# Kernel tuning notes

Measured on AMD Instinct MI355X. Metric: run time of the kernel, lower is better.

## Reference

```python
import jax, jax.numpy as jnp
import numpy as np

EPS = 1e-5
NEG = jnp.float32(-1e30)


def _mha(q_in, kv, in_w, in_b, out_w, out_b, n_heads, allowed=None):
    # torch nn.MultiheadAttention (batch_first, eval mode)
    B, Nq, D = q_in.shape
    hd = D // n_heads
    wq, wk, wv = jnp.split(in_w, 3, axis=0)
    bq, bk, bv = jnp.split(in_b, 3)
    q = (q_in @ wq.T + bq).reshape(B, Nq, n_heads, hd).transpose(0, 2, 1, 3)
    k = (kv @ wk.T + bk).reshape(B, -1, n_heads, hd).transpose(0, 2, 1, 3)
    v = (kv @ wv.T + bv).reshape(B, -1, n_heads, hd).transpose(0, 2, 1, 3)
    s = jnp.einsum('bhqd,bhkd->bhqk', q, k) / jnp.sqrt(jnp.float32(hd))
    if allowed is not None:
        s = jnp.where(allowed[:, None, :, :], s, NEG)
    a = jax.nn.softmax(s, axis=-1)
    o = jnp.einsum('bhqk,bhkd->bhqd', a, v).transpose(0, 2, 1, 3).reshape(B, Nq, D)
    o = o @ out_w.T + out_b
    if allowed is not None:
        # rows with no allowed keys: torch would NaN; we zero them (deterministic)
        o = jnp.where(allowed.any(-1)[..., None], o, 0.0)
    return o


def _layernorm(x, g, b):
    mu = x.mean(-1, keepdims=True)
    var = ((x - mu) ** 2).mean(-1, keepdims=True)
    return (x - mu) * jax.lax.rsqrt(var + EPS) * g + b


def setup_inputs() -> dict:
    key = jax.random.key(0)
    B, N, D, NH = 128, 128, 512, 8
    ks = jax.random.split(key, 16)
    s = 0.02
    return {
        'H': jax.random.normal(ks[0], (B, N, D), jnp.float32),
        'pred_heads': jax.random.randint(ks[1], (B, N), 0, N, jnp.int32),
        'mask': jnp.ones((B, N), jnp.int32),
        'head_in_w': jax.random.normal(ks[2], (3 * D, D)) * s,
        'head_in_b': jnp.zeros((3 * D,), jnp.float32),
        'head_out_w': jax.random.normal(ks[3], (D, D)) * s,
        'head_out_b': jnp.zeros((D,), jnp.float32),
        'sib_in_w': jax.random.normal(ks[4], (3 * D, D)) * s,
        'sib_in_b': jnp.zeros((3 * D,), jnp.float32),
        'sib_out_w': jax.random.normal(ks[5], (D, D)) * s,
        'sib_out_b': jnp.zeros((D,), jnp.float32),
        'child_w': jax.random.normal(ks[6], (D, 2 * D)) * s,
        'child_b': jnp.zeros((D,), jnp.float32),
        'gate_w': jax.random.normal(ks[7], (D, 4 * D)) * s,
        'gate_b': jnp.zeros((D,), jnp.float32),
        'trans_w': jax.random.normal(ks[8], (D, 4 * D)) * s,
        'trans_b': jnp.zeros((D,), jnp.float32),
        'ln_g': jnp.ones((D,), jnp.float32),
        'ln_b': jnp.zeros((D,), jnp.float32),
    }


def reference(H, pred_heads, mask, head_in_w, head_in_b, head_out_w, head_out_b,
              sib_in_w, sib_in_b, sib_out_w, sib_out_b, child_w, child_b,
              gate_w, gate_b, trans_w, trans_b, ln_g, ln_b):
    B, N, D = H.shape
    NH = 8
    heads = jnp.clip(pred_heads, 0, N - 1)  # [B,N]
    maskb = mask.astype(bool)

    # 1) head message: gather each node's head repr, attend Q=H, K=V=head_repr
    head_repr = jnp.take_along_axis(H, heads[..., None], axis=1)  # [B,N,D]
    head_msg = _mha(H, head_repr, head_in_w, head_in_b, head_out_w, head_out_b, NH)

    # 2) child aggregation: vectorized scatter-add replacing the Python loop.
    # loop runs d in [1, length) with mask a prefix -> valid = mask & (d >= 1)
    valid = maskb & (jnp.arange(N) >= 1)  # [B,N]
    contrib = H * valid[..., None].astype(H.dtype)
    flat_idx = (jnp.arange(B)[:, None] * N + heads).reshape(-1)
    child_sum = jnp.zeros((B * N, D), H.dtype).at[flat_idx].add(
        contrib.reshape(B * N, D)).reshape(B, N, D)
    child_count = jnp.zeros((B * N,), H.dtype).at[flat_idx].add(
        valid.reshape(-1).astype(H.dtype)).reshape(B, N, 1)
    child_avg = child_sum / jnp.maximum(child_count, 1.0)
    child_msg = jax.nn.gelu(
        jnp.concatenate([H, child_avg], -1) @ child_w.T + child_b,
        approximate=False)

    # 3) sibling attention (N <= 128 branch): same head, not self, both masked-in
    same_head = heads[:, :, None] == heads[:, None, :]
    eye = jnp.eye(N, dtype=bool)[None]
    allowed = same_head & ~eye & maskb[:, None, :] & maskb[:, :, None]
    sib_msg = _mha(H, H, sib_in_w, sib_in_b, sib_out_w, sib_out_b, NH, allowed=allowed)

    # 4) gated fusion + residual + layernorm
    combined = jnp.concatenate([H, head_msg, child_msg, sib_msg], -1)
    gate = jax.nn.sigmoid(combined @ gate_w.T + gate_b)
    update = jax.nn.gelu(combined @ trans_w.T + trans_b, approximate=False)
    return _layernorm(H + gate * update, ln_g, ln_b)
```

## Files before the change

### kernel.cpp

```cpp
#include <hip/hip_runtime.h>
#include <hip/hip_bf16.h>

typedef __bf16 bf16x8 __attribute__((ext_vector_type(8)));
typedef float f32x4 __attribute__((ext_vector_type(4)));

__device__ __forceinline__ void gload16(const void* g, void* l) {
  __builtin_amdgcn_global_load_lds(
      (const __attribute__((address_space(1))) unsigned int*)g,
      (__attribute__((address_space(3))) unsigned int*)l, 16, 0, 0);
}

__device__ __forceinline__ float gelu_f(float x) {
  return 0.5f * x * (1.f + erff(x * 0.70710678118654752f));
}
__device__ __forceinline__ float sigmoid_f(float x) {
  return 1.f / (1.f + __expf(-x));
}

template<int EPI>
__global__ __launch_bounds__(512, 2)
void gemm8_kernel(const __hip_bfloat16* __restrict__ A0, int lda0,
                  const __hip_bfloat16* __restrict__ A1, int lda1,
                  const __hip_bfloat16* __restrict__ A2, int lda2,
                  int ks1, int ks2,
                  const __hip_bfloat16* __restrict__ B, int ldb,
                  const float* __restrict__ bias,
                  const float* __restrict__ fvec,
                  const float* __restrict__ flags,
                  void* __restrict__ C, int ldc, int K)
{
  extern __shared__ __align__(16) char lds[];
  const int t = threadIdx.x;
  const int l = t & 63;
  const int w = t >> 6;
  const int l15 = l & 15, lg = (l >> 4) & 3;
  const int orig = blockIdx.y * gridDim.x + blockIdx.x;
  const int nwg = gridDim.x * gridDim.y;
  const int gy = gridDim.y;
  const int xcd = orig & 7, rk = orig >> 3, q = nwg >> 3, r = nwg & 7;
  const int bid = (xcd < r ? xcd * (q + 1) : r * (q + 1) + (xcd - r) * q) + rk;
  const int m0 = (bid % gy) * 256;
  const int n0 = (bid / gy) * 256;

  const int srow = t >> 2;
  const int kc8 = ((t & 3) ^ ((t >> 3) & 3)) * 8;
  const int mbase = (w >> 2) * 128;
  const int nbase = (w & 3) * 64;
  const int swz = (l15 >> 1) & 3;
  const int kslot = (lg ^ swz) * 8;
  int aoff[8], boff[4];
#pragma unroll
  for (int mf = 0; mf < 8; ++mf) aoff[mf] = (mbase + mf * 16 + l15) * 32 + kslot;
#pragma unroll
  for (int nf = 0; nf < 4; ++nf) boff[nf] = (nbase + nf * 16 + l15) * 32 + kslot;

  auto segA = [&](int k0, const __hip_bfloat16*& Ap, int& ldA, int& krel) {
    if (k0 >= ks2)      { Ap = A2; ldA = lda2; krel = k0 - ks2; }
    else if (k0 >= ks1) { Ap = A1; ldA = lda1; krel = k0 - ks1; }
    else                { Ap = A0; ldA = lda0; krel = k0; }
  };
  auto stageA = [&](int buf, const __hip_bfloat16* Ap, int ldA, int krel) {
    char* base = lds + buf * 32768 + t * 16;
    gload16(Ap + (size_t)(m0 + srow) * ldA + krel + kc8, base);
    gload16(Ap + (size_t)(m0 + 128 + srow) * ldA + krel + kc8, base + 8192);
  };
  auto stageB = [&](int buf, int k0) {
    char* base = lds + buf * 32768 + 16384 + t * 16;
    gload16(B + (size_t)(n0 + srow) * ldb + k0 + kc8, base);
    gload16(B + (size_t)(n0 + 128 + srow) * ldb + k0 + kc8, base + 8192);
  };

  f32x4 acc[8][4] = {};
  const int NT = K >> 5;

#pragma unroll 1
  for (int pt = 0; pt < 3; ++pt) {
    const __hip_bfloat16* Ap; int ldA, krel;
    segA(pt * 32, Ap, ldA, krel);
    stageA(pt, Ap, ldA, krel);
    stageB(pt, pt * 32);
  }
  asm volatile("s_waitcnt vmcnt(8)" ::: "memory");
  __builtin_amdgcn_s_barrier();
  __builtin_amdgcn_sched_barrier(0);

#pragma unroll 1
  for (int tt = 0; tt < NT; ++tt) {
    const int buf = tt & 3;
    const __hip_bfloat16* As = (const __hip_bfloat16*)(lds + buf * 32768);
    const __hip_bfloat16* Bs = (const __hip_bfloat16*)(lds + buf * 32768 + 16384);
    const int pf = tt + 3;
    const bool do_pf = pf < NT;
    const int pbuf = pf & 3;
    const __hip_bfloat16* Ap = A0; int ldA = lda0, krel = 0;
    if (do_pf) segA(pf * 32, Ap, ldA, krel);

    bf16x8 bv[4], av[4];
#pragma unroll
    for (int nf = 0; nf < 4; ++nf) bv[nf] = *(const bf16x8*)(Bs + boff[nf]);
#pragma unroll
    for (int mf = 0; mf < 4; ++mf) av[mf] = *(const bf16x8*)(As + aoff[mf]);
    if (do_pf) stageA(pbuf, Ap, ldA, krel);
    __builtin_amdgcn_s_setprio(1);
#pragma unroll
    for (int mf = 0; mf < 4; ++mf)
#pragma unroll
      for (int nf = 0; nf < 4; ++nf)
        acc[mf][nf] = __builtin_amdgcn_mfma_f32_16x16x32_bf16(av[mf], bv[nf], acc[mf][nf], 0, 0, 0);
    __builtin_amdgcn_s_setprio(0);

#pragma unroll
    for (int mf = 0; mf < 4; ++mf) av[mf] = *(const bf16x8*)(As + aoff[mf + 4]);
    if (do_pf) stageB(pbuf, pf * 32);
    __builtin_amdgcn_s_setprio(1);
#pragma unroll
    for (int mf = 0; mf < 4; ++mf)
#pragma unroll
      for (int nf = 0; nf < 4; ++nf)
        acc[mf + 4][nf] = __builtin_amdgcn_mfma_f32_16x16x32_bf16(av[mf], bv[nf], acc[mf + 4][nf], 0, 0, 0);
    __builtin_amdgcn_s_setprio(0);

    __builtin_amdgcn_sched_barrier(0);
    if (tt + 3 < NT)      asm volatile("s_waitcnt vmcnt(8)" ::: "memory");
    else if (tt + 2 < NT) asm volatile("s_waitcnt vmcnt(4)" ::: "memory");
    else if (tt + 1 < NT) asm volatile("s_waitcnt vmcnt(0)" ::: "memory");
    if (tt + 1 < NT) {
      __builtin_amdgcn_s_barrier();
      __builtin_amdgcn_sched_barrier(0);
    }
  }

  if (EPI == 2) {
#pragma unroll
    for (int mf = 0; mf < 8; ++mf) {
#pragma unroll
      for (int nh = 0; nh < 2; ++nh) {
        const int nf = nh * 2;
        const int sc = n0 + nbase + nf * 16;
        const float bg = bias[sc + l15], bt = bias[sc + 16 + l15];
        const float fg = fvec[sc + l15], ft = fvec[sc + 16 + l15];
        const int ocol = (sc >> 5) * 16 + l15;
#pragma unroll
        for (int j = 0; j < 4; ++j) {
          const int row = m0 + mbase + mf * 16 + lg * 4 + j;
          const float flg = flags[row];
          float g  = acc[mf][nf][j]     + bg + flg * fg;
          float tv = acc[mf][nf + 1][j] + bt + flg * ft;
          ((__hip_bfloat16*)C)[(size_t)row * ldc + ocol] =
              __float2bfloat16(sigmoid_f(g) * gelu_f(tv));
        }
      }
    }
    return;
  }
#pragma unroll
  for (int mf = 0; mf < 8; ++mf)
#pragma unroll
    for (int nf = 0; nf < 4; ++nf) {
      const int col = n0 + nbase + nf * 16 + l15;
      const float bc = bias ? bias[col] : 0.f;
#pragma unroll
      for (int j = 0; j < 4; ++j) {
        const int row = m0 + mbase + mf * 16 + lg * 4 + j;
        ((__hip_bfloat16*)C)[(size_t)row * ldc + col] =
            __float2bfloat16(acc[mf][nf][j] + bc);
      }
    }
}

template<int EPI, bool OBF16>
__global__ __launch_bounds__(256)
void gemm_kernel(const __hip_bfloat16* __restrict__ A0, int lda0,
                 const __hip_bfloat16* __restrict__ A1, int lda1,
                 const __hip_bfloat16* __restrict__ A2, int lda2,
                 int ks1, int ks2,
                 const __hip_bfloat16* __restrict__ B, int ldb,
                 const float* __restrict__ bias,
                 const float* __restrict__ fvec,
                 const float* __restrict__ flags,
                 void* __restrict__ C, int ldc, int K)
{
  __shared__ __align__(16) __hip_bfloat16 As[128 * 32];
  __shared__ __align__(16) __hip_bfloat16 Bs[128 * 32];
  const int t = threadIdx.x;
  const int l = t & 63, w = t >> 6;
  const int gx = gridDim.x;
  int bid = blockIdx.y * gx + blockIdx.x;
  {
    const int nwg = gx * gridDim.y;
    const int xcd = bid & 7, rk = bid >> 3, q = nwg >> 3, r = nwg & 7;
    bid = (xcd < r ? xcd * (q + 1) : r * (q + 1) + (xcd - r) * q) + rk;
  }
  const int m0 = (bid / gx) * 128, n0 = (bid % gx) * 128;
  const int wm = (w >> 1) * 64, wn = (w & 1) * 64;
  const int l15 = l & 15, lg = l >> 4;

  const int r0 = t >> 2;
  const int kk0 = ((t & 3) ^ ((t >> 3) & 3)) * 8;
  char* lA = (char*)As + t * 16;
  char* lB = (char*)Bs + t * 16;
  const size_t boff1 = (size_t)(n0 + r0) * ldb + kk0;
  const size_t boff2 = (size_t)(n0 + r0 + 64) * ldb + kk0;

  int aoffR[4], boffR[4];
#pragma unroll
  for (int i = 0; i < 4; ++i) {
    const int ra = wm + i * 16 + l15;
    aoffR[i] = ra * 32 + ((lg ^ ((ra >> 1) & 3)) * 8);
    const int rb = wn + i * 16 + l15;
    boffR[i] = rb * 32 + ((lg ^ ((rb >> 1) & 3)) * 8);
  }
  f32x4 acc[4][4] = {};

#pragma unroll 1
  for (int seg = 0; seg < 3; ++seg) {
    const __hip_bfloat16* Ap;
    int ldA, kb, ke;
    if (seg == 0)      { Ap = A0; ldA = lda0; kb = 0;   ke = ks1; }
    else if (seg == 1) { Ap = A1; ldA = lda1; kb = ks1; ke = ks2; }
    else               { Ap = A2; ldA = lda2; kb = ks2; ke = K;   }
    if (kb >= ke) continue;
    const size_t aoff1 = (size_t)(m0 + r0) * ldA + kk0;
    const size_t aoff2 = (size_t)(m0 + r0 + 64) * ldA + kk0;
    for (int k0 = kb; k0 < ke; k0 += 32) {
      const int kr = k0 - kb;
      gload16(Ap + aoff1 + kr, lA);
      gload16(Ap + aoff2 + kr, lA + 4096);
      gload16(B + boff1 + k0, lB);
      gload16(B + boff2 + k0, lB + 4096);
      __syncthreads();
      bf16x8 af[4], bfr[4];
#pragma unroll
      for (int i = 0; i < 4; ++i) {
        af[i]  = *(const bf16x8*)((const __hip_bfloat16*)As + aoffR[i]);
        bfr[i] = *(const bf16x8*)((const __hip_bfloat16*)Bs + boffR[i]);
      }
#pragma unroll
      for (int mi = 0; mi < 4; ++mi)
#pragma unroll
        for (int ni = 0; ni < 4; ++ni)
          acc[mi][ni] = __builtin_amdgcn_mfma_f32_16x16x32_bf16(af[mi], bfr[ni], acc[mi][ni], 0, 0, 0);
      __syncthreads();
    }
  }

#pragma unroll
  for (int mi = 0; mi < 4; ++mi)
#pragma unroll
    for (int ni = 0; ni < 4; ++ni) {
      const int col = n0 + wn + ni * 16 + l15;
      const float bc = bias ? bias[col] : 0.f;
#pragma unroll
      for (int j = 0; j < 4; ++j) {
        const int row = m0 + wm + mi * 16 + lg * 4 + j;
        float v = acc[mi][ni][j] + bc;
        if (EPI == 1) v = gelu_f(v);
        if (OBF16) ((__hip_bfloat16*)C)[(size_t)row * ldc + col] = __float2bfloat16(v);
        else       ((float*)C)[(size_t)row * ldc + col] = v;
      }
    }
}

__global__ __launch_bounds__(256)
void attn_kernel(const __hip_bfloat16* __restrict__ QKV,
                 const int* __restrict__ pred_heads,
                 const int* __restrict__ mask,
                 __hip_bfloat16* __restrict__ Oout,
                 float* __restrict__ flags)
{
  __shared__ __align__(16) __hip_bfloat16 smem[128 * 128];
  __shared__ __align__(16) __hip_bfloat16 Vt[64 * 128];
  __shared__ int hs[128];
  __shared__ int key[128];
  const bool SIB = blockIdx.x >= 1024;
  const int bh = blockIdx.x & 1023;
  const int b = bh >> 3, h = bh & 7;
  const int qofs = SIB ? 1536 : 0;
  __hip_bfloat16* Ob = Oout + (SIB ? 512 : 0);
  const int t = threadIdx.x, l = t & 63, w = t >> 6;
  const int l15 = l & 15, lg = l >> 4;
  __hip_bfloat16* Qs = smem;
  __hip_bfloat16* Ks = smem + 128 * 64;

  if (t < 128) {
    int hh = pred_heads[b * 128 + t];
    hh = hh < 0 ? 0 : (hh > 127 ? 127 : hh);
    hs[t] = hh;
    key[t] = mask[b * 128 + t] ? hh : (128 + t);
  }
  __syncthreads();
  const size_t tb = (size_t)b * 128 * 3072;
  const int co = qofs + h * 64;
#pragma unroll
  for (int it = 0; it < 4; ++it) {
    const int idx = it * 256 + t;
    const int row = idx >> 3;
    const int c8 = (idx & 7) * 8;
    const int sl = ((c8 >> 3) ^ (row & 7)) * 8;
    *(uint4*)(Qs + row * 64 + sl) = *(const uint4*)(QKV + tb + (size_t)row * 3072 + co + c8);
    const int krow = SIB ? row : hs[row];
    *(uint4*)(Ks + row * 64 + sl) = *(const uint4*)(QKV + tb + (size_t)krow * 3072 + co + 512 + c8);
    uint4 vv = *(const uint4*)(QKV + tb + (size_t)krow * 3072 + co + 1024 + c8);
    const __hip_bfloat16* vp = (const __hip_bfloat16*)&vv;
#pragma unroll
    for (int u = 0; u < 8; ++u) {
      const int d = c8 + u;
      Vt[d * 128 + (((row >> 3) ^ (d & 7)) * 8) + (row & 7)] = vp[u];
    }
  }
  __syncthreads();

  const int r0 = w * 32;
  const int x7 = l15 & 7;
  f32x4 s[8][2] = {};
#pragma unroll
  for (int ks = 0; ks < 2; ++ks) {
    const int sl = ((ks * 4 + lg) ^ x7) * 8;
    bf16x8 qb0 = *(const bf16x8*)(Qs + (r0 + l15) * 64 + sl);
    bf16x8 qb1 = *(const bf16x8*)(Qs + (r0 + 16 + l15) * 64 + sl);
#pragma unroll
    for (int kf = 0; kf < 8; ++kf) {
      bf16x8 ka = *(const bf16x8*)(Ks + (kf * 16 + l15) * 64 + sl);
      s[kf][0] = __builtin_amdgcn_mfma_f32_16x16x32_bf16(ka, qb0, s[kf][0], 0, 0, 0);
      s[kf][1] = __builtin_amdgcn_mfma_f32_16x16x32_bf16(ka, qb1, s[kf][1], 0, 0, 0);
    }
  }

  const float scale = 0.125f;
  int kq[2] = {0, 0};
  int4 kv[8];
  if (SIB) {
    kq[0] = key[r0 + l15];
    kq[1] = key[r0 + 16 + l15];
#pragma unroll
    for (int kf = 0; kf < 8; ++kf) kv[kf] = *(const int4*)&key[kf * 16 + lg * 4];
  }
  float invs[2];
#pragma unroll
  for (int qf = 0; qf < 2; ++qf) {
    const int q = r0 + qf * 16 + l15;
    unsigned om = 0xFFFFFFFFu;
    if (SIB) {
      om = 0u;
#pragma unroll
      for (int kf = 0; kf < 8; ++kf) {
        const int* kp = (const int*)&kv[kf];
#pragma unroll
        for (int j = 0; j < 4; ++j) {
          const int k = kf * 16 + lg * 4 + j;
          if (kp[j] == kq[qf] && k != q) om |= (1u << (kf * 4 + j));
        }
      }
    }
    float mx = -1e30f;
#pragma unroll
    for (int kf = 0; kf < 8; ++kf)
#pragma unroll
      for (int j = 0; j < 4; ++j) {
        const float v = s[kf][qf][j] * scale;
        mx = fmaxf(mx, ((om >> (kf * 4 + j)) & 1u) ? v : -1e30f);
      }
    mx = fmaxf(mx, __shfl_xor(mx, 16));
    mx = fmaxf(mx, __shfl_xor(mx, 32));
    float sum = 0.f;
#pragma unroll
    for (int kf = 0; kf < 8; ++kf)
#pragma unroll
      for (int j = 0; j < 4; ++j) {
        const float v = s[kf][qf][j] * scale;
        const float p = ((om >> (kf * 4 + j)) & 1u) ? __expf(v - mx) : 0.f;
        s[kf][qf][j] = p;
        sum += p;
      }
    sum += __shfl_xor(sum, 16);
    sum += __shfl_xor(sum, 32);
    invs[qf] = sum > 0.f ? 1.f / sum : 0.f;
  }
  if (SIB && h == 0 && lg == 0) {
    flags[b * 128 + r0 + l15]      = invs[0] > 0.f ? 1.f : 0.f;
    flags[b * 128 + r0 + 16 + l15] = invs[1] > 0.f ? 1.f : 0.f;
  }

  __syncthreads();
#pragma unroll
  for (int qf = 0; qf < 2; ++qf) {
    const int q = r0 + qf * 16 + l15;
    const int base = q * 128 + ((lg & 1) << 2);
#pragma unroll
    for (int kf = 0; kf < 8; ++kf) {
      const int c16 = kf * 2 + (lg >> 1);
      __hip_bfloat16 pk[4];
#pragma unroll
      for (int j = 0; j < 4; ++j) pk[j] = __float2bfloat16(s[kf][qf][j] * invs[qf]);
      *(uint2*)(smem + base + ((c16 ^ x7) << 3)) = *(const uint2*)pk;
    }
  }
  __syncthreads();

  f32x4 o[2][4] = {};
#pragma unroll
  for (int js = 0; js < 4; ++js) {
    const int slp = ((js * 4 + lg) ^ x7) * 8;
    bf16x8 pa0 = *(const bf16x8*)(smem + (r0 + l15) * 128 + slp);
    bf16x8 pa1 = *(const bf16x8*)(smem + (r0 + 16 + l15) * 128 + slp);
#pragma unroll
    for (int dj = 0; dj < 4; ++dj) {
      bf16x8 vb = *(const bf16x8*)(Vt + (dj * 16 + l15) * 128 + slp);
      o[0][dj] = __builtin_amdgcn_mfma_f32_16x16x32_bf16(pa0, vb, o[0][dj], 0, 0, 0);
      o[1][dj] = __builtin_amdgcn_mfma_f32_16x16x32_bf16(pa1, vb, o[1][dj], 0, 0, 0);
    }
  }
  const int hb = h * 64;
#pragma unroll
  for (int mi = 0; mi < 2; ++mi)
#pragma unroll
    for (int dj = 0; dj < 4; ++dj)
#pragma unroll
      for (int j = 0; j < 4; ++j) {
        const int row = r0 + mi * 16 + lg * 4 + j;
        const int dc = dj * 16 + l15;
        Ob[(size_t)(b * 128 + row) * 1024 + hb + dc] = __float2bfloat16(o[mi][dj][j]);
      }
}

__global__ __launch_bounds__(256)
void child_kernel(const __hip_bfloat16* __restrict__ Hbf,
                  const int* __restrict__ pred_heads,
                  const int* __restrict__ mask,
                  __hip_bfloat16* __restrict__ Cavg)
{
  __shared__ float sum[128 * 64];
  __shared__ int cnt[128];
  __shared__ int hsl[128];
  __shared__ int vld[128];
  const int t = threadIdx.x;
  const int b = blockIdx.y, ch = blockIdx.x;
#pragma unroll
  for (int u = 0; u < 32; ++u) sum[u * 256 + t] = 0.f;
  if (t < 128) {
    int hh = pred_heads[b * 128 + t];
    hh = hh < 0 ? 0 : (hh > 127 ? 127 : hh);
    hsl[t] = hh;
    vld[t] = (mask[b * 128 + t] != 0) && (t >= 1);
    cnt[t] = 0;
  }
  __syncthreads();
  if (t < 128 && vld[t]) atomicAdd(&cnt[hsl[t]], 1);
  __syncthreads();
  const int c = t & 63;
  const int isub = t >> 6;
  for (int ii = 0; ii < 32; ++ii) {
    int i = ii * 4 + isub;
    if (vld[i])
      atomicAdd(&sum[hsl[i] * 64 + c],
                __bfloat162float(Hbf[((size_t)b * 128 + i) * 512 + ch * 64 + c]));
  }
  __syncthreads();
#pragma unroll
  for (int u = 0; u < 32; ++u) {
    int idx = u * 256 + t;
    int p = idx >> 6, cc = idx & 63;
    float avg = sum[idx] / fmaxf((float)cnt[p], 1.f);
    Cavg[((size_t)b * 128 + p) * 512 + ch * 64 + cc] = __float2bfloat16(avg);
  }
}

__global__ void prep_kernel(const float* __restrict__ hin_w, const float* __restrict__ sin_w,
                            const float* __restrict__ ch_w, const float* __restrict__ H,
                            __hip_bfloat16* __restrict__ Wqkv, __hip_bfloat16* __restrict__ Wch,
                            __hip_bfloat16* __restrict__ Hbf,
                            const float* __restrict__ gw, const float* __restrict__ tw,
                            const float* __restrict__ gb, const float* __restrict__ tb,
                            __hip_bfloat16* __restrict__ Wf, __hip_bfloat16* __restrict__ Whin,
                            __hip_bfloat16* __restrict__ Wsin, float* __restrict__ bias,
                            const float* __restrict__ hout_w, const float* __restrict__ sout_w,
                            __hip_bfloat16* __restrict__ WhoT, __hip_bfloat16* __restrict__ WsoT)
{
  int gid = blockIdx.x * 256 + threadIdx.x;
  if (gid < 2621440) {
    const float* s; __hip_bfloat16* d; int i;
    if      (gid <  196608) { s = hin_w; d = Wqkv;          i = gid; }
    else if (gid <  393216) { s = sin_w; d = Wqkv + 786432; i = gid - 196608; }
    else if (gid <  524288) { s = ch_w;  d = Wch;           i = gid - 393216; }
    else                    { s = H;     d = Hbf;           i = gid - 524288; }
    i *= 4;
    float4 v = *(const float4*)(s + i);
    union { __hip_bfloat16 h[4]; uint2 u; } p;
    p.h[0] = __float2bfloat16(v.x); p.h[1] = __float2bfloat16(v.y);
    p.h[2] = __float2bfloat16(v.z); p.h[3] = __float2bfloat16(v.w);
    *(uint2*)(d + i) = p.u;
  } else if (gid < 4718592) {
    int idx = gid - 2621440;
    int s = idx >> 11, c = idx & 2047;
    int q = s >> 5, r = s & 31;
    float v = (r < 16) ? gw[(size_t)(q * 16 + r) * 2048 + c]
                       : tw[(size_t)(q * 16 + r - 16) * 2048 + c];
    __hip_bfloat16 hv = __float2bfloat16(v);
    if      (c <  512) Wf[(size_t)s * 2048 + c] = hv;
    else if (c < 1024) Whin[(size_t)s * 512 + (c - 512)] = hv;
    else if (c < 1536) Wf[(size_t)s * 2048 + (c - 512)] = hv;
    else               Wsin[(size_t)s * 512 + (c - 1536)] = hv;
    if (c == 0) bias[s] = (r < 16) ? gb[q * 16 + r] : tb[q * 16 + r - 16];
  } else {
    int idx = gid - 4718592;
    const float* s = hout_w; __hip_bfloat16* d = WhoT;
    if (idx >= 262144) { s = sout_w; d = WsoT; idx -= 262144; }
    int i = idx >> 9, j = idx & 511;
    d[i * 512 + j] = __float2bfloat16(s[(size_t)j * 512 + i]);
  }
}

__global__ __launch_bounds__(256)
void foldbias_kernel(const __hip_bfloat16* __restrict__ Whin, const __hip_bfloat16* __restrict__ Wsin,
                     const float* __restrict__ hob, const float* __restrict__ sob,
                     float* __restrict__ bias_gt, float* __restrict__ fvec)
{
  const int s = blockIdx.x * 256 + threadIdx.x;
  float a = 0.f, c = 0.f;
  for (int j = 0; j < 512; j += 8) {
    bf16x8 wh = *(const bf16x8*)(Whin + (size_t)s * 512 + j);
    bf16x8 wsv = *(const bf16x8*)(Wsin + (size_t)s * 512 + j);
#pragma unroll
    for (int u = 0; u < 8; ++u) {
      a += (float)wh[u] * hob[j + u];
      c += (float)wsv[u] * sob[j + u];
    }
  }
  bias_gt[s] += a;
  fvec[s] = c;
}

__global__ __launch_bounds__(64)
void ln_kernel(const float* __restrict__ H, const __hip_bfloat16* __restrict__ U,
               const float* __restrict__ g, const float* __restrict__ bta,
               float* __restrict__ out)
{
  const int row = blockIdx.x, l = threadIdx.x;
  const size_t hb = (size_t)row * 512;
  const int c0 = l * 8;
  float4 h0 = *(const float4*)(H + hb + c0);
  float4 h1 = *(const float4*)(H + hb + c0 + 4);
  bf16x8 uv = *(const bf16x8*)(U + hb + c0);
  float x[8];
  x[0] = h0.x + (float)uv[0]; x[1] = h0.y + (float)uv[1];
  x[2] = h0.z + (float)uv[2]; x[3] = h0.w + (float)uv[3];
  x[4] = h1.x + (float)uv[4]; x[5] = h1.y + (float)uv[5];
  x[6] = h1.z + (float)uv[6]; x[7] = h1.w + (float)uv[7];
  float sum = 0.f;
#pragma unroll
  for (int u = 0; u < 8; ++u) sum += x[u];
#pragma unroll
  for (int m = 32; m; m >>= 1) sum += __shfl_xor(sum, m);
  const float mean = sum * (1.f / 512.f);
  float vs = 0.f;
#pragma unroll
  for (int u = 0; u < 8; ++u) { float d0 = x[u] - mean; vs += d0 * d0; }
#pragma unroll
  for (int m = 32; m; m >>= 1) vs += __shfl_xor(vs, m);
  const float rstd = rsqrtf(vs * (1.f / 512.f) + 1e-5f);
  float4 g0 = *(const float4*)(g + c0);
  float4 g1 = *(const float4*)(g + c0 + 4);
  float4 b0 = *(const float4*)(bta + c0);
  float4 b1 = *(const float4*)(bta + c0 + 4);
  float4 o0, o1;
  o0.x = (x[0] - mean) * rstd * g0.x + b0.x;
  o0.y = (x[1] - mean) * rstd * g0.y + b0.y;
  o0.z = (x[2] - mean) * rstd * g0.z + b0.z;
  o0.w = (x[3] - mean) * rstd * g0.w + b0.w;
  o1.x = (x[4] - mean) * rstd * g1.x + b1.x;
  o1.y = (x[5] - mean) * rstd * g1.y + b1.y;
  o1.z = (x[6] - mean) * rstd * g1.z + b1.z;
  o1.w = (x[7] - mean) * rstd * g1.w + b1.w;
  *(float4*)(out + hb + c0) = o0;
  *(float4*)(out + hb + c0 + 4) = o1;
}

extern "C" void kernel_launch(void* const* d_in, const int* in_sizes, int n_in,
                              void* d_out, int out_size, void* d_ws, size_t ws_size,
                              hipStream_t stream)
{
  (void)in_sizes; (void)n_in; (void)out_size; (void)ws_size;
  const float* H      = (const float*)d_in[0];
  const int*  pred    = (const int*)d_in[1];
  const int*  maskp   = (const int*)d_in[2];
  const float* hin_w  = (const float*)d_in[3];
  const float* hin_b  = (const float*)d_in[4];
  const float* hout_w = (const float*)d_in[5];
  const float* hout_b = (const float*)d_in[6];
  const float* sin_w  = (const float*)d_in[7];
  const float* sin_b  = (const float*)d_in[8];
  const float* sout_w = (const float*)d_in[9];
  const float* sout_b = (const float*)d_in[10];
  const float* ch_w   = (const float*)d_in[11];
  const float* ch_b   = (const float*)d_in[12];
  const float* g_w    = (const float*)d_in[13];
  const float* g_b    = (const float*)d_in[14];
  const float* t_w    = (const float*)d_in[15];
  const float* t_b    = (const float*)d_in[16];
  const float* lng    = (const float*)d_in[17];
  const float* lnb    = (const float*)d_in[18];

  char* ws = (char*)d_ws;
  __hip_bfloat16* Wqkv  = (__hip_bfloat16*)(ws + 0);
  __hip_bfloat16* Wch   = (__hip_bfloat16*)(ws + 3145728);
  __hip_bfloat16* Wgt   = (__hip_bfloat16*)(ws + 4194304);
  float* bias_qkv       = (float*)(ws + 8388608);
  float* bias_gt        = (float*)(ws + 8400896);
  float* fvec           = (float*)(ws + 8404992);
  float* flags          = (float*)(ws + 8409088);
  __hip_bfloat16* Hbf   = (__hip_bfloat16*)(ws + 8474624);
  char* QKVr            = ws + 25251840;
  __hip_bfloat16* QKV   = (__hip_bfloat16*)QKVr;
  __hip_bfloat16* Whin  = (__hip_bfloat16*)(QKVr + 0);
  __hip_bfloat16* Wsin  = (__hip_bfloat16*)(QKVr + 1048576);
  __hip_bfloat16* WhoT  = (__hip_bfloat16*)(QKVr + 2097152);
  __hip_bfloat16* WsoT  = (__hip_bfloat16*)(QKVr + 2621440);
  __hip_bfloat16* CHM   = (__hip_bfloat16*)(QKVr + 0);
  __hip_bfloat16* U     = (__hip_bfloat16*)(QKVr + 16777216);
  __hip_bfloat16* Cavg  = (__hip_bfloat16*)(QKVr + 50331648);
  __hip_bfloat16* CM2   = (__hip_bfloat16*)(ws + 125915136);

  hipFuncSetAttribute(reinterpret_cast<const void*>(gemm8_kernel<0>),
                      hipFuncAttributeMaxDynamicSharedMemorySize, 131072);
  hipFuncSetAttribute(reinterpret_cast<const void*>(gemm8_kernel<2>),
                      hipFuncAttributeMaxDynamicSharedMemorySize, 131072);

  prep_kernel<<<20480, 256, 0, stream>>>(hin_w, sin_w, ch_w, H, Wqkv, Wch, Hbf,
                                         g_w, t_w, g_b, t_b, Wgt, Whin, Wsin, bias_gt,
                                         hout_w, sout_w, WhoT, WsoT);
  foldbias_kernel<<<4, 256, 0, stream>>>(Whin, Wsin, hout_b, sout_b, bias_gt, fvec);
  hipMemcpyAsync(bias_qkv, hin_b, 1536 * 4, hipMemcpyDeviceToDevice, stream);
  hipMemcpyAsync(bias_qkv + 1536, sin_b, 1536 * 4, hipMemcpyDeviceToDevice, stream);

  gemm_kernel<0, true><<<dim3(4, 8), 256, 0, stream>>>(
      Whin, 512, Whin, 512, Whin, 512, 512, 512, WhoT, 512,
      (const float*)nullptr, (const float*)nullptr, (const float*)nullptr,
      (void*)(Wgt + 1024), 2048, 512);
  gemm_kernel<0, true><<<dim3(4, 8), 256, 0, stream>>>(
      Wsin, 512, Wsin, 512, Wsin, 512, 512, 512, WsoT, 512,
      (const float*)nullptr, (const float*)nullptr, (const float*)nullptr,
      (void*)(Wgt + 1536), 2048, 512);

  gemm8_kernel<0><<<dim3(12, 64), 512, 131072, stream>>>(
      Hbf, 512, Hbf, 512, Hbf, 512, 512, 512, Wqkv, 512,
      bias_qkv, (const float*)nullptr, (const float*)nullptr,
      (void*)QKV, 3072, 512);

  attn_kernel<<<2048, 256, 0, stream>>>(QKV, pred, maskp, CM2, flags);

  child_kernel<<<dim3(8, 128), 256, 0, stream>>>(Hbf, pred, maskp, Cavg);
  gemm_kernel<1, true><<<dim3(4, 128), 256, 0, stream>>>(
      Hbf, 512, Cavg, 512, Cavg, 512, 512, 1024, Wch, 1024,
      ch_b, (const float*)nullptr, (const float*)nullptr,
      (void*)CHM, 512, 1024);

  gemm8_kernel<2><<<dim3(4, 64), 512, 131072, stream>>>(
      Hbf, 512, CHM, 512, CM2, 1024, 512, 1024, Wgt, 2048,
      bias_gt, fvec, flags, (void*)U, 512, 2048);

  ln_kernel<<<16384, 64, 0, stream>>>(H, U, lng, lnb, (float*)d_out);
}
```

Baseline: 453.9 us.

## Restructure GEMM main loop into 64-wide K double-buffer with staged half-tile prefetch

```diff
diff --git a/kernel.cpp b/kernel.cpp
--- a/kernel.cpp
+++ b/kernel.cpp
@@ -41,66 +41,66 @@
   const int bid = (xcd < r ? xcd * (q + 1) : r * (q + 1) + (xcd - r) * q) + rk;
   const int m0 = (bid % gy) * 256;
   const int n0 = (bid / gy) * 256;
-
-  const int srow = t >> 2;
-  const int kc8 = ((t & 3) ^ ((t >> 3) & 3)) * 8;
-  const int mbase = (w >> 2) * 128;
-  const int nbase = (w & 3) * 64;
-  const int swz = (l15 >> 1) & 3;
-  const int kslot = (lg ^ swz) * 8;
-  int aoff[8], boff[4];
-#pragma unroll
-  for (int mf = 0; mf < 8; ++mf) aoff[mf] = (mbase + mf * 16 + l15) * 32 + kslot;
-#pragma unroll
-  for (int nf = 0; nf < 4; ++nf) boff[nf] = (nbase + nf * 16 + l15) * 32 + kslot;
+  const int wm = w >> 2, wn = w & 3;
+
+  const int srow0 = t >> 2;
+  const int sch = ((t & 3) ^ ((t >> 2) & 3)) * 8;
 
   auto segA = [&](int k0, const __hip_bfloat16*& Ap, int& ldA, int& krel) {
     if (k0 >= ks2)      { Ap = A2; ldA = lda2; krel = k0 - ks2; }
     else if (k0 >= ks1) { Ap = A1; ldA = lda1; krel = k0 - ks1; }
     else                { Ap = A0; ldA = lda0; krel = k0; }
   };
-  auto stageA = [&](int buf, const __hip_bfloat16* Ap, int ldA, int krel) {
-    char* base = lds + buf * 32768 + t * 16;
-    gload16(Ap + (size_t)(m0 + srow) * ldA + krel + kc8, base);
-    gload16(Ap + (size_t)(m0 + 128 + srow) * ldA + krel + kc8, base + 8192);
+  auto stageA = [&](int U, int kh) {
+    const __hip_bfloat16* Ap; int ldA, krel;
+    segA(U * 64 + kh * 32, Ap, ldA, krel);
+    char* dst = lds + (U & 1) * 65536 + kh * 16384 + t * 16;
+    gload16(Ap + (size_t)(m0 + srow0) * ldA + krel + sch, dst);
+    gload16(Ap + (size_t)(m0 + 128 + srow0) * ldA + krel + sch, dst + 8192);
   };
-  auto stageB = [&](int buf, int k0) {
-    char* base = lds + buf * 32768 + 16384 + t * 16;
-    gload16(B + (size_t)(n0 + srow) * ldb + k0 + kc8, base);
-    gload16(B + (size_t)(n0 + 128 + srow) * ldb + k0 + kc8, base + 8192);
+  auto stageB = [&](int U, int kh) {
+    const int k0 = U * 64 + kh * 32;
+    char* dst = lds + (U & 1) * 65536 + 32768 + kh * 16384 + t * 16;
+    gload16(B + (size_t)(n0 + srow0) * ldb + k0 + sch, dst);
+    gload16(B + (size_t)(n0 + 128 + srow0) * ldb + k0 + sch, dst + 8192);
   };
 
+  const int key = l15 & 3;
+  const int kch = (lg ^ key) * 8;
+  int aoff[8], boff[4];
+#pragma unroll
+  for (int mf = 0; mf < 8; ++mf) aoff[mf] = (wm * 128 + mf * 16 + l15) * 32 + kch;
+#pragma unroll
+  for (int nf = 0; nf < 4; ++nf) boff[nf] = (wn * 64 + nf * 16 + l15) * 32 + kch;
+
   f32x4 acc[8][4] = {};
-  const int NT = K >> 5;
-
-#pragma unroll 1
-  for (int pt = 0; pt < 3; ++pt) {
-    const __hip_bfloat16* Ap; int ldA, krel;
-    segA(pt * 32, Ap, ldA, krel);
-    stageA(pt, Ap, ldA, krel);
-    stageB(pt, pt * 32);
-  }
-  asm volatile("s_waitcnt vmcnt(8)" ::: "memory");
+  const int NT = K >> 6;
+
+  stageA(0, 0); stageB(0, 0); stageA(0, 1); stageB(0, 1);
+  if (NT > 1) { stageA(1, 0); stageB(1, 0); }
+  if (NT > 1) asm volatile("s_waitcnt vmcnt(8)" ::: "memory");
+  else        asm volatile("s_waitcnt vmcnt(4)" ::: "memory");
   __builtin_amdgcn_s_barrier();
   __builtin_amdgcn_sched_barrier(0);
 
 #pragma unroll 1
-  for (int tt = 0; tt < NT; ++tt) {
-    const int buf = tt & 3;
-    const __hip_bfloat16* As = (const __hip_bfloat16*)(lds + buf * 32768);
-    const __hip_bfloat16* Bs = (const __hip_bfloat16*)(lds + buf * 32768 + 16384);
-    const int pf = tt + 3;
-    const bool do_pf = pf < NT;
-    const int pbuf = pf & 3;
-    const __hip_bfloat16* Ap = A0; int ldA = lda0, krel = 0;
-    if (do_pf) segA(pf * 32, Ap, ldA, krel);
-
-    bf16x8 bv[4], av[4];
-#pragma unroll
-    for (int nf = 0; nf < 4; ++nf) bv[nf] = *(const bf16x8*)(Bs + boff[nf]);
-#pragma unroll
-    for (int mf = 0; mf < 4; ++mf) av[mf] = *(const bf16x8*)(As + aoff[mf]);
-    if (do_pf) stageA(pbuf, Ap, ldA, krel);
+  for (int U = 0; U < NT; ++U) {
+    const int b = U & 1;
+    const __hip_bfloat16* RA0 = (const __hip_bfloat16*)(lds + b * 65536);
+    const __hip_bfloat16* RA1 = (const __hip_bfloat16*)(lds + b * 65536 + 16384);
+    const __hip_bfloat16* RB0 = (const __hip_bfloat16*)(lds + b * 65536 + 32768);
+    const __hip_bfloat16* RB1 = (const __hip_bfloat16*)(lds + b * 65536 + 49152);
+    bf16x8 av[4], bv[4];
+
+#pragma unroll
+    for (int mf = 0; mf < 4; ++mf) av[mf] = *(const bf16x8*)(RA0 + aoff[mf]);
+#pragma unroll
+    for (int nf = 0; nf < 4; ++nf) bv[nf] = *(const bf16x8*)(RB0 + boff[nf]);
+    __builtin_amdgcn_sched_barrier(0);
+    if (U + 1 < NT) stageA(U + 1, 1);
+    __builtin_amdgcn_s_barrier();
+    asm volatile("s_waitcnt lgkmcnt(0)" ::: "memory");
+    __builtin_amdgcn_sched_barrier(0);
     __builtin_amdgcn_s_setprio(1);
 #pragma unroll
     for (int mf = 0; mf < 4; ++mf)
@@ -108,10 +108,15 @@
       for (int nf = 0; nf < 4; ++nf)
         acc[mf][nf] = __builtin_amdgcn_mfma_f32_16x16x32_bf16(av[mf], bv[nf], acc[mf][nf], 0, 0, 0);
     __builtin_amdgcn_s_setprio(0);
-
-#pragma unroll
-    for (int mf = 0; mf < 4; ++mf) av[mf] = *(const bf16x8*)(As + aoff[mf + 4]);
-    if (do_pf) stageB(pbuf, pf * 32);
+    __builtin_amdgcn_s_barrier();
+
+#pragma unroll
+    for (int mf = 0; mf < 4; ++mf) av[mf] = *(const bf16x8*)(RA0 + aoff[mf + 4]);
+    __builtin_amdgcn_sched_barrier(0);
+    if (U + 1 < NT) stageB(U + 1, 1);
+    __builtin_amdgcn_s_barrier();
+    asm volatile("s_waitcnt lgkmcnt(0)" ::: "memory");
+    __builtin_amdgcn_sched_barrier(0);
     __builtin_amdgcn_s_setprio(1);
 #pragma unroll
     for (int mf = 0; mf < 4; ++mf)
@@ -119,17 +124,51 @@
       for (int nf = 0; nf < 4; ++nf)
         acc[mf + 4][nf] = __builtin_amdgcn_mfma_f32_16x16x32_bf16(av[mf], bv[nf], acc[mf + 4][nf], 0, 0, 0);
     __builtin_amdgcn_s_setprio(0);
-
-    __builtin_amdgcn_sched_barrier(0);
-    if (tt + 3 < NT)      asm volatile("s_waitcnt vmcnt(8)" ::: "memory");
-    else if (tt + 2 < NT) asm volatile("s_waitcnt vmcnt(4)" ::: "memory");
-    else if (tt + 1 < NT) asm volatile("s_waitcnt vmcnt(0)" ::: "memory");
-    if (tt + 1 < NT) {
-      __builtin_amdgcn_s_barrier();
-      __builtin_amdgcn_sched_barrier(0);
-    }
-  }
-
+    __builtin_amdgcn_sched_barrier(0);
+    if (U + 1 < NT) asm volatile("s_waitcnt vmcnt(8)" ::: "memory");
+    else            asm volatile("s_waitcnt vmcnt(0)" ::: "memory");
+    __builtin_amdgcn_s_barrier();
+
+#pragma unroll
+    for (int mf = 0; mf < 4; ++mf) av[mf] = *(const bf16x8*)(RA1 + aoff[mf]);
+#pragma unroll
+    for (int nf = 0; nf < 4; ++nf) bv[nf] = *(const bf16x8*)(RB1 + boff[nf]);
+    __builtin_amdgcn_sched_barrier(0);
+    if (U + 2 < NT) stageA(U + 2, 0);
+    __builtin_amdgcn_s_barrier();
+    asm volatile("s_waitcnt lgkmcnt(0)" ::: "memory");
+    __builtin_amdgcn_sched_barrier(0);
+    __builtin_amdgcn_s_setprio(1);
+#pragma unroll
+    for (int mf = 0; mf < 4; ++mf)
+#pragma unroll
+      for (int nf = 0; nf < 4; ++nf)
+        acc[mf][nf] = __builtin_amdgcn_mfma_f32_16x16x32_bf16(av[mf], bv[nf], acc[mf][nf], 0, 0, 0);
+    __builtin_amdgcn_s_setprio(0);
+    __builtin_amdgcn_s_barrier();
+
+#pragma unroll
+    for (int mf = 0; mf < 4; ++mf) av[mf] = *(const bf16x8*)(RA1 + aoff[mf + 4]);
+    __builtin_amdgcn_sched_barrier(0);
+    if (U + 2 < NT) stageB(U + 2, 0);
+    __builtin_amdgcn_s_barrier();
+    asm volatile("s_waitcnt lgkmcnt(0)" ::: "memory");
+    __builtin_amdgcn_sched_barrier(0);
+    __builtin_amdgcn_s_setprio(1);
+#pragma unroll
+    for (int mf = 0; mf < 4; ++mf)
+#pragma unroll
+      for (int nf = 0; nf < 4; ++nf)
+        acc[mf + 4][nf] = __builtin_amdgcn_mfma_f32_16x16x32_bf16(av[mf], bv[nf], acc[mf + 4][nf], 0, 0, 0);
+    __builtin_amdgcn_s_setprio(0);
+    __builtin_amdgcn_sched_barrier(0);
+    if (U + 2 < NT)      asm volatile("s_waitcnt vmcnt(8)" ::: "memory");
+    else if (U + 1 < NT) asm volatile("s_waitcnt vmcnt(4)" ::: "memory");
+    __builtin_amdgcn_s_barrier();
+  }
+
+  const int mbase = wm * 128;
+  const int nbase = wn * 64;
   if (EPI == 2) {
 #pragma unroll
     for (int mf = 0; mf < 8; ++mf) {
```

Measured after the change: 471.9 us. 1.04x slower.
